# Optimization experiments

Hardware: AMD Instinct MI355X
Metric: run time of the kernel (lower is better)

## Reference

```python
import jax, jax.numpy as jnp
import numpy as np

B, C, G = 16384, 30, 7  # YOLOv1: 2 boxes*5 + 20 classes = 30 channels, 7x7 grid


def setup_inputs() -> dict:
    key = jax.random.key(0)
    k1, k2, k3 = jax.random.split(key, 3)
    pred = jax.random.uniform(k1, (B, C, G, G), dtype=jnp.float32)
    labels = jax.random.uniform(k2, (B, C, G, G), dtype=jnp.float32)
    # objectness indicator must be exactly 0.0 or 1.0 (source tests == 1)
    obj = (jax.random.uniform(k3, (B, G, G)) < 0.15).astype(jnp.float32)
    labels = labels.at[:, 4].set(obj)
    return {"pred": pred, "labels": labels}


def _xyxy(px, py, w, h, gx, gy, M, N):
    # (px,py) are cell-relative centers; grid index m along dim -2, n along dim -1
    cx = (px + gx) / M
    cy = (py + gy) / N
    return cx - w / 2, cy - h / 2, cx + w / 2, cy + h / 2


def _iou(a, b):
    x1 = jnp.maximum(a[0], b[0])
    y1 = jnp.maximum(a[1], b[1])
    x2 = jnp.minimum(a[2], b[2])
    y2 = jnp.minimum(a[3], b[3])
    inter = jnp.clip(x2 - x1, 0.0) * jnp.clip(y2 - y1, 0.0)
    area_a = (a[2] - a[0]) * (a[3] - a[1])
    area_b = (b[2] - b[0]) * (b[3] - b[1])
    return jnp.where(inter > 0, inter / (area_a + area_b - inter), 0.0)


def reference(pred, labels):
    M, N = labels.shape[-2], labels.shape[-1]  # num_gridx, num_gridy
    gx = jnp.arange(M, dtype=pred.dtype)[:, None]  # m index (dim -2)
    gy = jnp.arange(N, dtype=pred.dtype)[None, :]  # n index (dim -1)

    b1 = _xyxy(pred[:, 0], pred[:, 1], pred[:, 2], pred[:, 3], gx, gy, M, N)
    b2 = _xyxy(pred[:, 5], pred[:, 6], pred[:, 7], pred[:, 8], gx, gy, M, N)
    bg = _xyxy(labels[:, 0], labels[:, 1], labels[:, 2], labels[:, 3], gx, gy, M, N)

    iou1 = _iou(b1, bg)  # [B, G, G]
    iou2 = _iou(b2, bg)
    resp1 = iou1 > iou2

    obj = (labels[:, 4] == 1.0).astype(pred.dtype)  # [B, G, G]

    coor1 = (jnp.sum((pred[:, 0:2] - labels[:, 0:2]) ** 2, axis=1)
             + jnp.sum((jnp.sqrt(pred[:, 2:4]) - jnp.sqrt(labels[:, 2:4])) ** 2, axis=1))
    coor2 = (jnp.sum((pred[:, 5:7] - labels[:, 5:7]) ** 2, axis=1)
             + jnp.sum((jnp.sqrt(pred[:, 7:9]) - jnp.sqrt(labels[:, 7:9])) ** 2, axis=1))
    coor = jnp.where(resp1, coor1, coor2)

    obj_conf = jnp.where(resp1, (pred[:, 4] - iou1) ** 2, (pred[:, 9] - iou2) ** 2)
    noobj_resp = jnp.where(resp1, (pred[:, 9] - iou2) ** 2, (pred[:, 4] - iou1) ** 2)
    cls = jnp.sum((pred[:, 10:] - labels[:, 10:]) ** 2, axis=1)

    coor_loss = 5.0 * jnp.sum(coor * obj)
    obj_confi_loss = jnp.sum(obj_conf * obj)
    noobj_confi_loss = (0.5 * jnp.sum(noobj_resp * obj)
                        + 0.5 * jnp.sum((pred[:, 4] ** 2 + pred[:, 9] ** 2) * (1.0 - obj)))
    class_loss = jnp.sum(cls * obj)

    loss = coor_loss + obj_confi_loss + noobj_confi_loss + class_loss
    # NOTE: the source shadows `n` (batch size) with the inner grid loop variable,
    # so the final division is by range(7)[-1] == 6, NOT by batch size. Faithful:
    return loss / (N - 1)
```

## Files before the change

kernel.cpp:

```cpp
#include <hip/hip_runtime.h>


constexpr int BATCH = 16384;
constexpr int CH    = 30;
constexpr int G     = 7;
constexpr int GG    = G * G;
constexpr int CELLS = BATCH * GG;
constexpr int TPB   = 256;
constexpr int NBLK  = CELLS / TPB;

__global__ void zero_out_kernel(float* __restrict__ out) {
    out[0] = 0.0f;
}

__device__ __forceinline__ float sq(float x) { return x * x; }

__global__ __launch_bounds__(TPB) void yolo_loss_kernel(
    const float* __restrict__ pred,
    const float* __restrict__ lab,
    float* __restrict__ out)
{
    const int tid  = blockIdx.x * TPB + threadIdx.x;
    const int b    = tid / GG;
    const int cell = tid - b * GG;
    const int m    = cell / G;
    const int n    = cell - m * G;

    const float* p = pred + (size_t)b * (CH * GG) + cell;
    const float* l = lab  + (size_t)b * (CH * GG) + cell;

    float pv[10];
#pragma unroll
    for (int c = 0; c < 10; ++c) pv[c] = p[c * GG];
    float lv[9];
#pragma unroll
    for (int c = 0; c < 9; ++c) lv[c] = l[c * GG];

    float cls = 0.0f;
#pragma unroll
    for (int c = 10; c < 30; ++c) {
        float d = p[c * GG] - l[c * GG];
        cls += d * d;
    }

    const float gx = (float)m;
    const float gy = (float)n;
    const float inv7 = 1.0f / 7.0f;

    const float cx1 = (pv[0] + gx) * inv7, cy1 = (pv[1] + gy) * inv7;
    const float hw1 = 0.5f * pv[2],        hh1 = 0.5f * pv[3];
    const float a1x1 = cx1 - hw1, a1y1 = cy1 - hh1, a1x2 = cx1 + hw1, a1y2 = cy1 + hh1;
    const float cx2 = (pv[5] + gx) * inv7, cy2 = (pv[6] + gy) * inv7;
    const float hw2 = 0.5f * pv[7],        hh2 = 0.5f * pv[8];
    const float a2x1 = cx2 - hw2, a2y1 = cy2 - hh2, a2x2 = cx2 + hw2, a2y2 = cy2 + hh2;
    const float cxg = (lv[0] + gx) * inv7, cyg = (lv[1] + gy) * inv7;
    const float hwg = 0.5f * lv[2],        hhg = 0.5f * lv[3];
    const float gx1 = cxg - hwg, gy1 = cyg - hhg, gx2 = cxg + hwg, gy2 = cyg + hhg;

    const float area_g = (gx2 - gx1) * (gy2 - gy1);

    float ix1 = fmaxf(a1x1, gx1), iy1 = fmaxf(a1y1, gy1);
    float ix2 = fminf(a1x2, gx2), iy2 = fminf(a1y2, gy2);
    float inter1 = fmaxf(ix2 - ix1, 0.0f) * fmaxf(iy2 - iy1, 0.0f);
    float area1  = (a1x2 - a1x1) * (a1y2 - a1y1);
    float iou1 = (inter1 > 0.0f) ? inter1 / (area1 + area_g - inter1) : 0.0f;

    ix1 = fmaxf(a2x1, gx1); iy1 = fmaxf(a2y1, gy1);
    ix2 = fminf(a2x2, gx2); iy2 = fminf(a2y2, gy2);
    float inter2 = fmaxf(ix2 - ix1, 0.0f) * fmaxf(iy2 - iy1, 0.0f);
    float area2  = (a2x2 - a2x1) * (a2y2 - a2y1);
    float iou2 = (inter2 > 0.0f) ? inter2 / (area2 + area_g - inter2) : 0.0f;

    const bool resp1 = iou1 > iou2;
    const float obj = (lv[4] == 1.0f) ? 1.0f : 0.0f;

    const float coor1 = sq(pv[0] - lv[0]) + sq(pv[1] - lv[1])
                      + sq(sqrtf(pv[2]) - sqrtf(lv[2])) + sq(sqrtf(pv[3]) - sqrtf(lv[3]));
    const float coor2 = sq(pv[5] - lv[5]) + sq(pv[6] - lv[6])
                      + sq(sqrtf(pv[7]) - sqrtf(lv[7])) + sq(sqrtf(pv[8]) - sqrtf(lv[8]));
    const float coor = resp1 ? coor1 : coor2;

    const float e1 = sq(pv[4] - iou1);
    const float e2 = sq(pv[9] - iou2);
    const float obj_conf   = resp1 ? e1 : e2;
    const float noobj_resp = resp1 ? e2 : e1;

    float cell_loss = obj * (5.0f * coor + obj_conf + 0.5f * noobj_resp + cls)
                    + (1.0f - obj) * 0.5f * (pv[4] * pv[4] + pv[9] * pv[9]);

    float v = cell_loss;
#pragma unroll
    for (int off = 32; off > 0; off >>= 1) v += __shfl_down(v, off, 64);

    __shared__ float wsum[TPB / 64];
    const int lane = threadIdx.x & 63;
    const int wid  = threadIdx.x >> 6;
    if (lane == 0) wsum[wid] = v;
    __syncthreads();
    if (threadIdx.x == 0) {
        float s = wsum[0] + wsum[1] + wsum[2] + wsum[3];
        atomicAdd(out, s * (1.0f / 6.0f));
    }
}

extern "C" void kernel_launch(void* const* d_in, const int* in_sizes, int n_in,
                              void* d_out, int out_size, void* d_ws, size_t ws_size,
                              hipStream_t stream) {
    const float* pred = (const float*)d_in[0];
    const float* lab  = (const float*)d_in[1];
    float* out = (float*)d_out;

    zero_out_kernel<<<1, 1, 0, stream>>>(out);
    yolo_loss_kernel<<<NBLK, TPB, 0, stream>>>(pred, lab, out);
}
```

Before: 209.8 us.

## Stage per-image tiles via coalesced float4 loads into LDS; two-pass reduction

Each block now loads 4 whole images of pred and labels with coalesced float4 global loads into shared memory, then 196 threads compute per-cell losses from LDS instead of issuing strided scalar global loads. The per-block atomicAdd and zero kernel are replaced by writing partial sums to workspace and a single-block final reduction kernel. This trades fully coalesced vector traffic for ~47KB LDS per block (limiting occupancy) and 60 of 256 threads idling during compute.

```diff
diff --git a/kernel.cpp b/kernel.cpp
--- a/kernel.cpp
+++ b/kernel.cpp
@@ -1,105 +1,162 @@
 #include <hip/hip_runtime.h>
 
 
-constexpr int BATCH = 16384;
-constexpr int CH    = 30;
-constexpr int G     = 7;
-constexpr int GG    = G * G;
-constexpr int CELLS = BATCH * GG;
-constexpr int TPB   = 256;
-constexpr int NBLK  = CELLS / TPB;
-
-__global__ void zero_out_kernel(float* __restrict__ out) {
-    out[0] = 0.0f;
-}
+constexpr int BATCH  = 16384;
+constexpr int CH     = 30;
+constexpr int G      = 7;
+constexpr int GG     = G * G;
+constexpr int TPB    = 256;
+constexpr int IPB    = 4;
+constexpr int IMG_F  = CH * GG;
+constexpr int BLK_F  = IPB * IMG_F;
+constexpr int BLK_V4 = BLK_F / 4;
+constexpr int NBLK   = BATCH / IPB;
+constexpr int FULL_IT = BLK_V4 / TPB;
+constexpr int TAIL    = BLK_V4 - FULL_IT * TPB;
 
 __device__ __forceinline__ float sq(float x) { return x * x; }
 
-__global__ __launch_bounds__(TPB) void yolo_loss_kernel(
+__global__ __launch_bounds__(TPB) void yolo_loss_partial(
     const float* __restrict__ pred,
     const float* __restrict__ lab,
-    float* __restrict__ out)
+    float* __restrict__ ws)
 {
-    const int tid  = blockIdx.x * TPB + threadIdx.x;
-    const int b    = tid / GG;
-    const int cell = tid - b * GG;
-    const int m    = cell / G;
-    const int n    = cell - m * G;
+    __shared__ float4 sp4[BLK_V4];
+    __shared__ float4 sl4[BLK_V4];
+    __shared__ float wsum[TPB / 64];
 
-    const float* p = pred + (size_t)b * (CH * GG) + cell;
-    const float* l = lab  + (size_t)b * (CH * GG) + cell;
+    const int t = threadIdx.x;
+    const float4* gp = (const float4*)(pred + (size_t)blockIdx.x * BLK_F);
+    const float4* gl = (const float4*)(lab  + (size_t)blockIdx.x * BLK_F);
 
-    float pv[10];
+    float4 rp[FULL_IT + 1], rl[FULL_IT + 1];
 #pragma unroll
-    for (int c = 0; c < 10; ++c) pv[c] = p[c * GG];
-    float lv[9];
+    for (int j = 0; j < FULL_IT; ++j) {
+        rp[j] = gp[t + j * TPB];
+        rl[j] = gl[t + j * TPB];
+    }
+    const bool tail = t < TAIL;
+    if (tail) {
+        rp[FULL_IT] = gp[t + FULL_IT * TPB];
+        rl[FULL_IT] = gl[t + FULL_IT * TPB];
+    }
 #pragma unroll
-    for (int c = 0; c < 9; ++c) lv[c] = l[c * GG];
+    for (int j = 0; j < FULL_IT; ++j) {
+        sp4[t + j * TPB] = rp[j];
+        sl4[t + j * TPB] = rl[j];
+    }
+    if (tail) {
+        sp4[t + FULL_IT * TPB] = rp[FULL_IT];
+        sl4[t + FULL_IT * TPB] = rl[FULL_IT];
+    }
+    __syncthreads();
 
-    float cls = 0.0f;
+    const float* sp = (const float*)sp4;
+    const float* sl = (const float*)sl4;
+
+    float cell_loss = 0.0f;
+    if (t < IPB * GG) {
+        const int img  = t / GG;
+        const int cell = t - img * GG;
+        const int m    = cell / G;
+        const int n    = cell - m * G;
+
+        const float* p = sp + img * IMG_F + cell;
+        const float* l = sl + img * IMG_F + cell;
+
+        float pv[10];
 #pragma unroll
-    for (int c = 10; c < 30; ++c) {
-        float d = p[c * GG] - l[c * GG];
-        cls += d * d;
+        for (int c = 0; c < 10; ++c) pv[c] = p[c * GG];
+        float lv[9];
+#pragma unroll
+        for (int c = 0; c < 9; ++c) lv[c] = l[c * GG];
+
+        float cls = 0.0f;
+#pragma unroll
+        for (int c = 10; c < 30; ++c) {
+            float d = p[c * GG] - l[c * GG];
+            cls += d * d;
+        }
+
+        const float gx = (float)m;
+        const float gy = (float)n;
+        const float inv7 = 1.0f / 7.0f;
+
+        const float cx1 = (pv[0] + gx) * inv7, cy1 = (pv[1] + gy) * inv7;
+        const float hw1 = 0.5f * pv[2],        hh1 = 0.5f * pv[3];
+        const float a1x1 = cx1 - hw1, a1y1 = cy1 - hh1, a1x2 = cx1 + hw1, a1y2 = cy1 + hh1;
+        const float cx2 = (pv[5] + gx) * inv7, cy2 = (pv[6] + gy) * inv7;
+        const float hw2 = 0.5f * pv[7],        hh2 = 0.5f * pv[8];
+        const float a2x1 = cx2 - hw2, a2y1 = cy2 - hh2, a2x2 = cx2 + hw2, a2y2 = cy2 + hh2;
+        const float cxg = (lv[0] + gx) * inv7, cyg = (lv[1] + gy) * inv7;
+        const float hwg = 0.5f * lv[2],        hhg = 0.5f * lv[3];
+        const float bx1 = cxg - hwg, by1 = cyg - hhg, bx2 = cxg + hwg, by2 = cyg + hhg;
+
+        const float area_g = (bx2 - bx1) * (by2 - by1);
+
+        float ix1 = fmaxf(a1x1, bx1), iy1 = fmaxf(a1y1, by1);
+        float ix2 = fminf(a1x2, bx2), iy2 = fminf(a1y2, by2);
+        float inter1 = fmaxf(ix2 - ix1, 0.0f) * fmaxf(iy2 - iy1, 0.0f);
+        float area1  = (a1x2 - a1x1) * (a1y2 - a1y1);
+        float iou1 = (inter1 > 0.0f) ? inter1 / (area1 + area_g - inter1) : 0.0f;
+
+        ix1 = fmaxf(a2x1, bx1); iy1 = fmaxf(a2y1, by1);
+        ix2 = fminf(a2x2, bx2); iy2 = fminf(a2y2, by2);
+        float inter2 = fmaxf(ix2 - ix1, 0.0f) * fmaxf(iy2 - iy1, 0.0f);
+        float area2  = (a2x2 - a2x1) * (a2y2 - a2y1);
+        float iou2 = (inter2 > 0.0f) ? inter2 / (area2 + area_g - inter2) : 0.0f;
+
+        const bool resp1 = iou1 > iou2;
+        const float obj = (lv[4] == 1.0f) ? 1.0f : 0.0f;
+
+        const float coor1 = sq(pv[0] - lv[0]) + sq(pv[1] - lv[1])
+                          + sq(sqrtf(pv[2]) - sqrtf(lv[2])) + sq(sqrtf(pv[3]) - sqrtf(lv[3]));
+        const float coor2 = sq(pv[5] - lv[5]) + sq(pv[6] - lv[6])
+                          + sq(sqrtf(pv[7]) - sqrtf(lv[7])) + sq(sqrtf(pv[8]) - sqrtf(lv[8]));
+        const float coor = resp1 ? coor1 : coor2;
+
+        const float e1 = sq(pv[4] - iou1);
+        const float e2 = sq(pv[9] - iou2);
+        const float obj_conf   = resp1 ? e1 : e2;
+        const float noobj_resp = resp1 ? e2 : e1;
+
+        cell_loss = obj * (5.0f * coor + obj_conf + 0.5f * noobj_resp + cls)
+                  + (1.0f - obj) * 0.5f * (pv[4] * pv[4] + pv[9] * pv[9]);
     }
-
-    const float gx = (float)m;
-    const float gy = (float)n;
-    const float inv7 = 1.0f / 7.0f;
-
-    const float cx1 = (pv[0] + gx) * inv7, cy1 = (pv[1] + gy) * inv7;
-    const float hw1 = 0.5f * pv[2],        hh1 = 0.5f * pv[3];
-    const float a1x1 = cx1 - hw1, a1y1 = cy1 - hh1, a1x2 = cx1 + hw1, a1y2 = cy1 + hh1;
-    const float cx2 = (pv[5] + gx) * inv7, cy2 = (pv[6] + gy) * inv7;
-    const float hw2 = 0.5f * pv[7],        hh2 = 0.5f * pv[8];
-    const float a2x1 = cx2 - hw2, a2y1 = cy2 - hh2, a2x2 = cx2 + hw2, a2y2 = cy2 + hh2;
-    const float cxg = (lv[0] + gx) * inv7, cyg = (lv[1] + gy) * inv7;
-    const float hwg = 0.5f * lv[2],        hhg = 0.5f * lv[3];
-    const float gx1 = cxg - hwg, gy1 = cyg - hhg, gx2 = cxg + hwg, gy2 = cyg + hhg;
-
-    const float area_g = (gx2 - gx1) * (gy2 - gy1);
-
-    float ix1 = fmaxf(a1x1, gx1), iy1 = fmaxf(a1y1, gy1);
-    float ix2 = fminf(a1x2, gx2), iy2 = fminf(a1y2, gy2);
-    float inter1 = fmaxf(ix2 - ix1, 0.0f) * fmaxf(iy2 - iy1, 0.0f);
-    float area1  = (a1x2 - a1x1) * (a1y2 - a1y1);
-    float iou1 = (inter1 > 0.0f) ? inter1 / (area1 + area_g - inter1) : 0.0f;
-
-    ix1 = fmaxf(a2x1, gx1); iy1 = fmaxf(a2y1, gy1);
-    ix2 = fminf(a2x2, gx2); iy2 = fminf(a2y2, gy2);
-    float inter2 = fmaxf(ix2 - ix1, 0.0f) * fmaxf(iy2 - iy1, 0.0f);
-    float area2  = (a2x2 - a2x1) * (a2y2 - a2y1);
-    float iou2 = (inter2 > 0.0f) ? inter2 / (area2 + area_g - inter2) : 0.0f;
-
-    const bool resp1 = iou1 > iou2;
-    const float obj = (lv[4] == 1.0f) ? 1.0f : 0.0f;
-
-    const float coor1 = sq(pv[0] - lv[0]) + sq(pv[1] - lv[1])
-                      + sq(sqrtf(pv[2]) - sqrtf(lv[2])) + sq(sqrtf(pv[3]) - sqrtf(lv[3]));
-    const float coor2 = sq(pv[5] - lv[5]) + sq(pv[6] - lv[6])
-                      + sq(sqrtf(pv[7]) - sqrtf(lv[7])) + sq(sqrtf(pv[8]) - sqrtf(lv[8]));
-    const float coor = resp1 ? coor1 : coor2;
-
-    const float e1 = sq(pv[4] - iou1);
-    const float e2 = sq(pv[9] - iou2);
-    const float obj_conf   = resp1 ? e1 : e2;
-    const float noobj_resp = resp1 ? e2 : e1;
-
-    float cell_loss = obj * (5.0f * coor + obj_conf + 0.5f * noobj_resp + cls)
-                    + (1.0f - obj) * 0.5f * (pv[4] * pv[4] + pv[9] * pv[9]);
 
     float v = cell_loss;
 #pragma unroll
     for (int off = 32; off > 0; off >>= 1) v += __shfl_down(v, off, 64);
 
-    __shared__ float wsum[TPB / 64];
-    const int lane = threadIdx.x & 63;
-    const int wid  = threadIdx.x >> 6;
+    const int lane = t & 63;
+    const int wid  = t >> 6;
     if (lane == 0) wsum[wid] = v;
     __syncthreads();
-    if (threadIdx.x == 0) {
-        float s = wsum[0] + wsum[1] + wsum[2] + wsum[3];
-        atomicAdd(out, s * (1.0f / 6.0f));
+    if (t == 0) ws[blockIdx.x] = wsum[0] + wsum[1] + wsum[2] + wsum[3];
+}
+
+__global__ __launch_bounds__(TPB) void yolo_loss_final(
+    const float* __restrict__ ws, float* __restrict__ out)
+{
+    const int t = threadIdx.x;
+    const float4* w4 = (const float4*)ws;
+    float4 a = make_float4(0.f, 0.f, 0.f, 0.f);
+#pragma unroll
+    for (int j = 0; j < NBLK / 4 / TPB; ++j) {
+        float4 x = w4[t + j * TPB];
+        a.x += x.x; a.y += x.y; a.z += x.z; a.w += x.w;
+    }
+    float v = (a.x + a.y) + (a.z + a.w);
+#pragma unroll
+    for (int off = 32; off > 0; off >>= 1) v += __shfl_down(v, off, 64);
+
+    __shared__ float wsum[TPB / 64];
+    const int lane = t & 63;
+    const int wid  = t >> 6;
+    if (lane == 0) wsum[wid] = v;
+    __syncthreads();
+    if (t == 0) {
+        out[0] = (wsum[0] + wsum[1] + wsum[2] + wsum[3]) * (1.0f / 6.0f);
     }
 }
 
@@ -108,8 +165,9 @@
                               hipStream_t stream) {
     const float* pred = (const float*)d_in[0];
     const float* lab  = (const float*)d_in[1];
+    float* ws  = (float*)d_ws;
     float* out = (float*)d_out;
 
-    zero_out_kernel<<<1, 1, 0, stream>>>(out);
-    yolo_loss_kernel<<<NBLK, TPB, 0, stream>>>(pred, lab, out);
+    yolo_loss_partial<<<NBLK, TPB, 0, stream>>>(pred, lab, ws);
+    yolo_loss_final<<<1, TPB, 0, stream>>>(ws, out);
 }
```

New measurement: 229.3 us. 9.3% more time.
